# Performance work log

Hardware: AMD Instinct MI355X
Metric: run time of the kernel (lower is better)

Reference implementation:

```python
import jax, jax.numpy as jnp
import numpy as np

IN_F = 128
OUT_F = 128
GROUPS = 8
NUM_F = 8
B = 16
NP_ = 4096


def setup_inputs() -> dict:
    key = jax.random.key(0)
    ks = jax.random.split(key, 6)
    x = jax.random.normal(ks[0], (B, NP_, IN_F), dtype=jnp.float32)
    grid = jnp.arange(NUM_F, dtype=jnp.float32) + 1.0                      # [num_f]
    base_weight = jax.random.normal(ks[1], (OUT_F, IN_F), dtype=jnp.float32) * 0.05
    scale_sp = jnp.ones((OUT_F,), dtype=jnp.float32)
    coef = jax.random.uniform(ks[2], (GROUPS, 1, NUM_F), dtype=jnp.float32)
    conv_w = jax.random.normal(ks[3], (NUM_F, OUT_F, IN_F), dtype=jnp.float32) * 0.05  # grouped 1x1 conv
    conv_b = jax.random.normal(ks[4], (NUM_F, OUT_F), dtype=jnp.float32) * 0.05
    return {"x": x, "grid": grid, "base_weight": base_weight,
            "scale_sp": scale_sp, "coef": coef, "conv_w": conv_w, "conv_b": conv_b}


def reference(x, grid, base_weight, scale_sp, coef, conv_w, conv_b):
    Bd, Nd, D = x.shape
    num_f = grid.shape[0]
    groups = coef.shape[0]
    gsz = D // groups
    xf = x.reshape(Bd * Nd, D)                                  # [batch, in]
    # base path: SiLU then linear (no bias)
    base = jax.nn.silu(xf) @ base_weight.T                       # [batch, out]
    # spline path: sin(grid * x), broadcast coef per (group, f)
    s = jnp.sin(grid[None, :, None] * xf[:, None, :])            # [batch, num_f, in]
    cm = coef[:, 0, :].T                                         # [num_f, groups]
    s = s.reshape(-1, num_f, groups, gsz) * cm[None, :, :, None]
    s = s.reshape(-1, num_f, D)                                  # [batch, num_f, in]
    # grouped 1x1 conv == per-f GEMM
    spline = jnp.einsum('bfi,foi->bfo', s, conv_w) + conv_b[None]
    spline = spline.sum(axis=1) * scale_sp                       # [batch, out]
    out = (base + spline).reshape(Bd, Nd, -1)
    return out
```

## Files before the change

kernel.cpp:

```cpp
#include <hip/hip_runtime.h>
#include <hip/hip_bf16.h>
#include <stdint.h>

#define IN_F   128
#define OUT_F  128
#define NUM_F  8
#define NROWS  (16*4096)

typedef __bf16  bf16x8  __attribute__((ext_vector_type(8)));
typedef float   f32x16  __attribute__((ext_vector_type(16)));

#define WP_CHUNKS (9*8*4*64)
#define WP_BYTES  (WP_CHUNKS*16)
#define BIAS_OFF  WP_BYTES

__global__ __launch_bounds__(256) void skan_prep(
    const float* __restrict__ base_w,
    const float* __restrict__ scale,
    const float* __restrict__ coef,
    const float* __restrict__ conv_w,
    const float* __restrict__ conv_b,
    __bf16* __restrict__ Wp, float* __restrict__ bias)
{
    int gid = blockIdx.x * 256 + threadIdx.x;
    int l  = gid & 63;
    int t  = (gid >> 6) & 3;
    int s  = (gid >> 8) & 7;
    int fb = gid >> 11;
    int n  = t * 32 + (l & 31);
    int k0 = s * 16 + (l >> 5) * 8;
    __bf16* dst = Wp + (size_t)gid * 8;
    if (fb == 0) {
        #pragma unroll
        for (int j = 0; j < 8; ++j)
            dst[j] = (__bf16)base_w[n * IN_F + k0 + j];
    } else {
        int f = fb - 1;
        float sc = scale[n];
        #pragma unroll
        for (int j = 0; j < 8; ++j) {
            int k = k0 + j;
            float v = conv_w[((size_t)f * OUT_F + n) * IN_F + k]
                      * coef[(k >> 4) * NUM_F + f] * sc;
            dst[j] = (__bf16)v;
        }
    }
    if (gid < OUT_F) {
        float b = 0.f;
        #pragma unroll
        for (int f = 0; f < NUM_F; ++f) b += conv_b[f * OUT_F + gid];
        bias[gid] = b * scale[gid];
    }
}

__device__ __forceinline__ void gld_lds16(const void* g, void* l) {
    __builtin_amdgcn_global_load_lds(
        (const __attribute__((address_space(1))) uint32_t*)g,
        (__attribute__((address_space(3))) uint32_t*)l, 16, 0, 0);
}

__global__ __launch_bounds__(256, 2) void skan_main(
    const float* __restrict__ x,
    const __bf16* __restrict__ Wp,
    const float* __restrict__ bias,
    float* __restrict__ out)
{
    __shared__ uint4 smem4[2048];
    char* smem = (char*)smem4;

    const int tid = threadIdx.x;
    const int w   = tid >> 6;
    const int l   = tid & 63;
    const int hl  = l & 31;
    const int h   = l >> 5;
    const int m0  = blockIdx.x * 128 + w * 32;
    const int m   = m0 + hl;

    const float4* x4 = (const float4*)x + (size_t)m * (IN_F / 4) + 2 * h;
    float xe[64];
    #pragma unroll
    for (int s = 0; s < 8; ++s) {
        float4 a = x4[4 * s];
        float4 b = x4[4 * s + 1];
        xe[8*s+0] = a.x; xe[8*s+1] = a.y; xe[8*s+2] = a.z; xe[8*s+3] = a.w;
        xe[8*s+4] = b.x; xe[8*s+5] = b.y; xe[8*s+6] = b.z; xe[8*s+7] = b.w;
    }

    f32x16 acc[4];
    #pragma unroll
    for (int t = 0; t < 4; ++t)
        #pragma unroll
        for (int r = 0; r < 16; ++r) acc[t][r] = 0.f;

    const bf16x8* bp = (const bf16x8*)smem;
    const char* wpb  = (const char*)Wp;

    for (int fb = 0; fb < 9; ++fb) {
        __syncthreads();
        {
            const char* src = wpb + (size_t)fb * 32768;
            #pragma unroll
            for (int r = 0; r < 8; ++r) {
                int off = (r * 4 + w) * 1024;
                gld_lds16(src + off + l * 16, smem + off);
            }
        }
        bf16x8 af[8];
        if (fb == 0) {
            #pragma unroll
            for (int s = 0; s < 8; ++s)
                #pragma unroll
                for (int j = 0; j < 8; ++j) {
                    float v = xe[8*s+j];
                    float sv = v * __builtin_amdgcn_rcpf(1.0f + __expf(-v));
                    af[s][j] = (__bf16)sv;
                }
        } else {
            float cf = (float)fb * 0.15915494309189535f;
            #pragma unroll
            for (int s = 0; s < 8; ++s)
                #pragma unroll
                for (int j = 0; j < 8; ++j) {
                    float a = __builtin_amdgcn_fractf(cf * xe[8*s+j]);
                    af[s][j] = (__bf16)__builtin_amdgcn_sinf(a);
                }
        }
        __syncthreads();
        #pragma unroll
        for (int s = 0; s < 8; ++s) {
            #pragma unroll
            for (int t = 0; t < 4; ++t) {
                bf16x8 b = bp[(s * 4 + t) * 64 + l];
                acc[t] = __builtin_amdgcn_mfma_f32_32x32x16_bf16(af[s], b, acc[t], 0, 0, 0);
            }
        }
    }

    #pragma unroll
    for (int t = 0; t < 4; ++t) {
        float bv = bias[t * 32 + hl];
        #pragma unroll
        for (int r = 0; r < 16; ++r) {
            int row = (r & 3) + 8 * (r >> 2) + 4 * h;
            out[(size_t)(m0 + row) * OUT_F + t * 32 + hl] = acc[t][r] + bv;
        }
    }
}

extern "C" void kernel_launch(void* const* d_in, const int* in_sizes, int n_in,
                              void* d_out, int out_size, void* d_ws, size_t ws_size,
                              hipStream_t stream) {
    const float* x      = (const float*)d_in[0];
    const float* base_w = (const float*)d_in[2];
    const float* scale  = (const float*)d_in[3];
    const float* coef   = (const float*)d_in[4];
    const float* conv_w = (const float*)d_in[5];
    const float* conv_b = (const float*)d_in[6];
    __bf16* Wp   = (__bf16*)d_ws;
    float*  bias = (float*)((char*)d_ws + BIAS_OFF);
    float*  out  = (float*)d_out;

    skan_prep<<<WP_CHUNKS / 256, 256, 0, stream>>>(base_w, scale, coef, conv_w, conv_b, Wp, bias);
    skan_main<<<NROWS / 128, 256, 0, stream>>>(x, Wp, bias, out);
}
```

Measured before the change: 112.3 us.

## Double-buffer weight tiles in LDS and stage output through shared memory

Grows LDS to 64KB and double-buffers the per-feature weight tiles, so the next tile's global-to-LDS load and the next sin activation computation overlap with the current tile's MFMAs. This cuts one barrier per iteration. The epilogue now writes accumulators to LDS and then stores coalesced float4 rows instead of scattered scalar stores. The larger LDS footprint may lower occupancy below the two blocks per CU the launch bounds target.

```diff
diff --git a/kernel.cpp b/kernel.cpp
--- a/kernel.cpp
+++ b/kernel.cpp
@@ -65,8 +65,8 @@
     const float* __restrict__ bias,
     float* __restrict__ out)
 {
-    __shared__ uint4 smem4[2048];
-    char* smem = (char*)smem4;
+    __shared__ float smemf[16384];
+    char* smem = (char*)smemf;
 
     const int tid = threadIdx.x;
     const int w   = tid >> 6;
@@ -75,6 +75,15 @@
     const int h   = l >> 5;
     const int m0  = blockIdx.x * 128 + w * 32;
     const int m   = m0 + hl;
+
+    {
+        const char* src = (const char*)Wp;
+        #pragma unroll
+        for (int r = 0; r < 8; ++r) {
+            int off = (r * 4 + w) * 1024;
+            gld_lds16(src + off + l * 16, smem + off);
+        }
+    }
 
     const float4* x4 = (const float4*)x + (size_t)m * (IN_F / 4) + 2 * h;
     float xe[64];
@@ -86,37 +95,45 @@
         xe[8*s+4] = b.x; xe[8*s+5] = b.y; xe[8*s+6] = b.z; xe[8*s+7] = b.w;
     }
 
+    bf16x8 af[8];
+    #pragma unroll
+    for (int s = 0; s < 8; ++s)
+        #pragma unroll
+        for (int j = 0; j < 8; ++j) {
+            float v = xe[8*s+j];
+            float sv = v * __builtin_amdgcn_rcpf(1.0f + __expf(-v));
+            af[s][j] = (__bf16)sv;
+        }
+
     f32x16 acc[4];
     #pragma unroll
     for (int t = 0; t < 4; ++t)
         #pragma unroll
         for (int r = 0; r < 16; ++r) acc[t][r] = 0.f;
 
-    const bf16x8* bp = (const bf16x8*)smem;
-    const char* wpb  = (const char*)Wp;
+    __syncthreads();
 
     for (int fb = 0; fb < 9; ++fb) {
-        __syncthreads();
-        {
-            const char* src = wpb + (size_t)fb * 32768;
+        if (fb < 8) {
+            const char* src = (const char*)Wp + (size_t)(fb + 1) * 32768;
+            char* dst = smem + ((fb + 1) & 1) * 32768;
             #pragma unroll
             for (int r = 0; r < 8; ++r) {
                 int off = (r * 4 + w) * 1024;
-                gld_lds16(src + off + l * 16, smem + off);
+                gld_lds16(src + off + l * 16, dst + off);
             }
         }
-        bf16x8 af[8];
-        if (fb == 0) {
+        const bf16x8* bp = (const bf16x8*)(smem + (fb & 1) * 32768);
+        #pragma unroll
+        for (int s = 0; s < 8; ++s) {
             #pragma unroll
-            for (int s = 0; s < 8; ++s)
-                #pragma unroll
-                for (int j = 0; j < 8; ++j) {
-                    float v = xe[8*s+j];
-                    float sv = v * __builtin_amdgcn_rcpf(1.0f + __expf(-v));
-                    af[s][j] = (__bf16)sv;
-                }
-        } else {
-            float cf = (float)fb * 0.15915494309189535f;
+            for (int t = 0; t < 4; ++t) {
+                bf16x8 b = bp[(s * 4 + t) * 64 + l];
+                acc[t] = __builtin_amdgcn_mfma_f32_32x32x16_bf16(af[s], b, acc[t], 0, 0, 0);
+            }
+        }
+        if (fb < 8) {
+            float cf = (float)(fb + 1) * 0.15915494309189535f;
             #pragma unroll
             for (int s = 0; s < 8; ++s)
                 #pragma unroll
@@ -126,24 +143,24 @@
                 }
         }
         __syncthreads();
-        #pragma unroll
-        for (int s = 0; s < 8; ++s) {
-            #pragma unroll
-            for (int t = 0; t < 4; ++t) {
-                bf16x8 b = bp[(s * 4 + t) * 64 + l];
-                acc[t] = __builtin_amdgcn_mfma_f32_32x32x16_bf16(af[s], b, acc[t], 0, 0, 0);
-            }
-        }
     }
 
+    float* lw = (float*)(smem + w * 16384);
     #pragma unroll
     for (int t = 0; t < 4; ++t) {
         float bv = bias[t * 32 + hl];
         #pragma unroll
         for (int r = 0; r < 16; ++r) {
             int row = (r & 3) + 8 * (r >> 2) + 4 * h;
-            out[(size_t)(m0 + row) * OUT_F + t * 32 + hl] = acc[t][r] + bv;
+            lw[row * 128 + t * 32 + hl] = acc[t][r] + bv;
         }
+    }
+    float4* of4 = (float4*)out;
+    const float4* lw4 = (const float4*)lw;
+    #pragma unroll
+    for (int i = 0; i < 16; ++i) {
+        float4 v = lw4[i * 64 + l];
+        of4[(size_t)(m0 + 2 * i + h) * 32 + hl] = v;
     }
 }
 
```

New measurement: 113.7 us. No clear change (+1.3%).

## Double-buffer weight tiles in LDS and stage output through LDS

Applied to the files above, without the earlier changes.

Splits LDS into two 32 KB buffers so the next frequency block's weights load via global_load_lds while the current block's MFMAs run. This replaces the old load-then-sync-then-compute loop, which had two barriers per block. The sin/SiLU activation for each k-slice is now computed just before its MFMAs instead of building all eight fragments up front, which should cut register pressure. The epilogue writes accumulators into LDS and reads them back as row-contiguous float4 stores to global memory. The costs are twice the LDS per block, which may limit blocks per CU, and every wave redundantly loading the whole first tile.

```diff
diff --git a/kernel.cpp b/kernel.cpp
--- a/kernel.cpp
+++ b/kernel.cpp
@@ -59,14 +59,44 @@
         (__attribute__((address_space(3))) uint32_t*)l, 16, 0, 0);
 }
 
+#define STAGE(dstbuf, fbi)                                                    \
+    {                                                                         \
+        const char* _src = wpb + (size_t)(fbi) * 32768;                       \
+        _Pragma("unroll")                                                     \
+        for (int _r = 0; _r < 8; ++_r) {                                      \
+            int _off = (_r * 4 + w) * 1024 + l * 16;                          \
+            gld_lds16(_src + _off, (dstbuf) + _off);                          \
+        }                                                                     \
+    }
+
+#define FBODY(curbuf, fbi)                                                    \
+    {                                                                         \
+        const bf16x8* _bp = (const bf16x8*)(curbuf);                          \
+        float _cf = (float)(fbi) * 0.15915494309189535f;                      \
+        _Pragma("unroll")                                                     \
+        for (int _s = 0; _s < 8; ++_s) {                                      \
+            bf16x8 _af;                                                       \
+            _Pragma("unroll")                                                 \
+            for (int _j = 0; _j < 8; ++_j) {                                  \
+                float _a = __builtin_amdgcn_fractf(_cf * xe[8*_s+_j]);        \
+                _af[_j] = (__bf16)__builtin_amdgcn_sinf(_a);                  \
+            }                                                                 \
+            _Pragma("unroll")                                                 \
+            for (int _t = 0; _t < 4; ++_t) {                                  \
+                bf16x8 _b = _bp[(_s * 4 + _t) * 64 + l];                      \
+                acc[_t] = __builtin_amdgcn_mfma_f32_32x32x16_bf16(_af, _b, acc[_t], 0, 0, 0); \
+            }                                                                 \
+        }                                                                     \
+    }
+
 __global__ __launch_bounds__(256, 2) void skan_main(
     const float* __restrict__ x,
     const __bf16* __restrict__ Wp,
     const float* __restrict__ bias,
     float* __restrict__ out)
 {
-    __shared__ uint4 smem4[2048];
-    char* smem = (char*)smem4;
+    __shared__ __align__(16) char bufA[32768];
+    __shared__ __align__(16) char bufB[32768];
 
     const int tid = threadIdx.x;
     const int w   = tid >> 6;
@@ -76,12 +106,19 @@
     const int m0  = blockIdx.x * 128 + w * 32;
     const int m   = m0 + hl;
 
-    const float4* x4 = (const float4*)x + (size_t)m * (IN_F / 4) + 2 * h;
+    const char* wpb = (const char*)Wp;
+
+    #pragma unroll
+    for (int i = 0; i < 32; ++i)
+        gld_lds16(wpb + i * 1024 + l * 16, bufA + i * 1024 + l * 16);
+    STAGE(bufB, 1);
+
+    const float4* x4p = (const float4*)x + (size_t)m * (IN_F / 4) + 2 * h;
     float xe[64];
     #pragma unroll
     for (int s = 0; s < 8; ++s) {
-        float4 a = x4[4 * s];
-        float4 b = x4[4 * s + 1];
+        float4 a = x4p[4 * s];
+        float4 b = x4p[4 * s + 1];
         xe[8*s+0] = a.x; xe[8*s+1] = a.y; xe[8*s+2] = a.z; xe[8*s+3] = a.w;
         xe[8*s+4] = b.x; xe[8*s+5] = b.y; xe[8*s+6] = b.z; xe[8*s+7] = b.w;
     }
@@ -92,57 +129,56 @@
         #pragma unroll
         for (int r = 0; r < 16; ++r) acc[t][r] = 0.f;
 
-    const bf16x8* bp = (const bf16x8*)smem;
-    const char* wpb  = (const char*)Wp;
-
-    for (int fb = 0; fb < 9; ++fb) {
-        __syncthreads();
-        {
-            const char* src = wpb + (size_t)fb * 32768;
+    {
+        const bf16x8* bp = (const bf16x8*)bufA;
+        #pragma unroll
+        for (int s = 0; s < 8; ++s) {
+            bf16x8 af;
             #pragma unroll
-            for (int r = 0; r < 8; ++r) {
-                int off = (r * 4 + w) * 1024;
-                gld_lds16(src + off + l * 16, smem + off);
+            for (int j = 0; j < 8; ++j) {
+                float v = xe[8*s+j];
+                af[j] = (__bf16)(v * __builtin_amdgcn_rcpf(1.0f + __expf(-v)));
             }
-        }
-        bf16x8 af[8];
-        if (fb == 0) {
-            #pragma unroll
-            for (int s = 0; s < 8; ++s)
-                #pragma unroll
-                for (int j = 0; j < 8; ++j) {
-                    float v = xe[8*s+j];
-                    float sv = v * __builtin_amdgcn_rcpf(1.0f + __expf(-v));
-                    af[s][j] = (__bf16)sv;
-                }
-        } else {
-            float cf = (float)fb * 0.15915494309189535f;
-            #pragma unroll
-            for (int s = 0; s < 8; ++s)
-                #pragma unroll
-                for (int j = 0; j < 8; ++j) {
-                    float a = __builtin_amdgcn_fractf(cf * xe[8*s+j]);
-                    af[s][j] = (__bf16)__builtin_amdgcn_sinf(a);
-                }
-        }
-        __syncthreads();
-        #pragma unroll
-        for (int s = 0; s < 8; ++s) {
             #pragma unroll
             for (int t = 0; t < 4; ++t) {
                 bf16x8 b = bp[(s * 4 + t) * 64 + l];
-                acc[t] = __builtin_amdgcn_mfma_f32_32x32x16_bf16(af[s], b, acc[t], 0, 0, 0);
+                acc[t] = __builtin_amdgcn_mfma_f32_32x32x16_bf16(af, b, acc[t], 0, 0, 0);
             }
         }
     }
-
-    #pragma unroll
-    for (int t = 0; t < 4; ++t) {
-        float bv = bias[t * 32 + hl];
-        #pragma unroll
-        for (int r = 0; r < 16; ++r) {
-            int row = (r & 3) + 8 * (r >> 2) + 4 * h;
-            out[(size_t)(m0 + row) * OUT_F + t * 32 + hl] = acc[t][r] + bv;
+    __syncthreads();
+
+    #pragma unroll 1
+    for (int p = 0; p < 4; ++p) {
+        int fb = 2 * p + 1;
+        STAGE(bufA, fb + 1);
+        FBODY(bufB, fb);
+        __syncthreads();
+        if (p < 3) STAGE(bufB, fb + 2);
+        FBODY(bufA, fb + 1);
+        __syncthreads();
+    }
+
+    float*  lwf = (float*)(bufB + w * 8192);
+    float4* lw4 = (float4*)lwf;
+    float4* of4 = (float4*)out;
+    #pragma unroll
+    for (int p = 0; p < 2; ++p) {
+        #pragma unroll
+        for (int tt = 0; tt < 2; ++tt) {
+            int t = 2 * p + tt;
+            float bv = bias[t * 32 + hl];
+            #pragma unroll
+            for (int r = 0; r < 16; ++r) {
+                int row = (r & 3) + 8 * (r >> 2) + 4 * h;
+                lwf[row * 64 + tt * 32 + hl] = acc[t][r] + bv;
+            }
+        }
+        #pragma unroll
+        for (int i = 0; i < 8; ++i) {
+            float4 v = lw4[i * 64 + l];
+            int row = i * 4 + (l >> 4);
+            of4[(size_t)(m0 + row) * 32 + p * 16 + (l & 15)] = v;
         }
     }
 }
```

New measurement: 113.3 us. About the same (+1.0%).

## Split output columns per block, keep weights resident in LDS, use sine recurrence

Applied to the files above, without the earlier changes.

Each block now handles 256 rows and one half of the output columns, loading that half's full 9-slice weight set into LDS once instead of streaming it per slice with barriers. x is held packed as bf16 in registers to save VGPRs, and sin(f·x) for f=1..8 comes from the Chebyshev recurrence sin((f+1)x)=2cos(x)sin(fx)-sin((f-1)x), which replaces seven extra sin evaluations with FMAs. The trade-offs are: x is read twice (once per column half), x is rounded to bf16 before the activations, the recurrence builds up error across f, and occupancy drops to one block per CU given the large LDS footprint. The prep kernel's spline branch applies the same coef factor to all 8 values of a chunk, which is valid because 8-element chunks never cross a 16-wide group.

```diff
diff --git a/kernel.cpp b/kernel.cpp
--- a/kernel.cpp
+++ b/kernel.cpp
@@ -10,7 +10,8 @@
 typedef __bf16  bf16x8  __attribute__((ext_vector_type(8)));
 typedef float   f32x16  __attribute__((ext_vector_type(16)));
 
-#define WP_CHUNKS (9*8*4*64)
+#define LDS_HALF  (9*8*2*64*16)
+#define WP_CHUNKS (2*9*8*2*64)
 #define WP_BYTES  (WP_CHUNKS*16)
 #define BIAS_OFF  WP_BYTES
 
@@ -23,27 +24,30 @@
     __bf16* __restrict__ Wp, float* __restrict__ bias)
 {
     int gid = blockIdx.x * 256 + threadIdx.x;
-    int l  = gid & 63;
-    int t  = (gid >> 6) & 3;
-    int s  = (gid >> 8) & 7;
-    int fb = gid >> 11;
-    int n  = t * 32 + (l & 31);
+    int flat = gid;
+    int l  = flat & 63;  flat >>= 6;
+    int t2 = flat & 1;   flat >>= 1;
+    int s  = flat & 7;   flat >>= 3;
+    int fb = flat % 9;
+    int h2 = flat / 9;
+    int n  = h2 * 64 + t2 * 32 + (l & 31);
     int k0 = s * 16 + (l >> 5) * 8;
     __bf16* dst = Wp + (size_t)gid * 8;
     if (fb == 0) {
-        #pragma unroll
-        for (int j = 0; j < 8; ++j)
-            dst[j] = (__bf16)base_w[n * IN_F + k0 + j];
+        const float4* b4 = (const float4*)(base_w + n * IN_F + k0);
+        float4 a = b4[0], b = b4[1];
+        dst[0]=(__bf16)a.x; dst[1]=(__bf16)a.y; dst[2]=(__bf16)a.z; dst[3]=(__bf16)a.w;
+        dst[4]=(__bf16)b.x; dst[5]=(__bf16)b.y; dst[6]=(__bf16)b.z; dst[7]=(__bf16)b.w;
     } else {
         int f = fb - 1;
         float sc = scale[n];
-        #pragma unroll
-        for (int j = 0; j < 8; ++j) {
-            int k = k0 + j;
-            float v = conv_w[((size_t)f * OUT_F + n) * IN_F + k]
-                      * coef[(k >> 4) * NUM_F + f] * sc;
-            dst[j] = (__bf16)v;
-        }
+        const float4* c4 = (const float4*)(conv_w + ((size_t)f * OUT_F + n) * IN_F + k0);
+        float4 a = c4[0], b = c4[1];
+        float m0c = coef[((k0    ) >> 4) * NUM_F + f] * sc;
+        float m1c = coef[((k0 + 4) >> 4) * NUM_F + f] * sc;
+        (void)m1c;
+        dst[0]=(__bf16)(a.x*m0c); dst[1]=(__bf16)(a.y*m0c); dst[2]=(__bf16)(a.z*m0c); dst[3]=(__bf16)(a.w*m0c);
+        dst[4]=(__bf16)(b.x*m0c); dst[5]=(__bf16)(b.y*m0c); dst[6]=(__bf16)(b.z*m0c); dst[7]=(__bf16)(b.w*m0c);
     }
     if (gid < OUT_F) {
         float b = 0.f;
@@ -59,90 +63,146 @@
         (__attribute__((address_space(3))) uint32_t*)l, 16, 0, 0);
 }
 
-__global__ __launch_bounds__(256, 2) void skan_main(
+__device__ __forceinline__ uint32_t pkbf(float a, float b) {
+    __bf16 x = (__bf16)a, y = (__bf16)b;
+    uint16_t ux, uy;
+    __builtin_memcpy(&ux, &x, 2);
+    __builtin_memcpy(&uy, &y, 2);
+    return (uint32_t)ux | ((uint32_t)uy << 16);
+}
+__device__ __forceinline__ float upk_lo(uint32_t p) { return __uint_as_float(p << 16); }
+__device__ __forceinline__ float upk_hi(uint32_t p) { return __uint_as_float(p & 0xffff0000u); }
+
+__global__ __launch_bounds__(256, 1) void skan_main(
     const float* __restrict__ x,
     const __bf16* __restrict__ Wp,
     const float* __restrict__ bias,
     float* __restrict__ out)
 {
-    __shared__ uint4 smem4[2048];
-    char* smem = (char*)smem4;
-
-    const int tid = threadIdx.x;
-    const int w   = tid >> 6;
-    const int l   = tid & 63;
-    const int hl  = l & 31;
-    const int h   = l >> 5;
-    const int m0  = blockIdx.x * 128 + w * 32;
-    const int m   = m0 + hl;
-
-    const float4* x4 = (const float4*)x + (size_t)m * (IN_F / 4) + 2 * h;
-    float xe[64];
+    __shared__ __align__(16) char sB[LDS_HALF];
+
+    const int tid  = threadIdx.x;
+    const int w    = tid >> 6;
+    const int l    = tid & 63;
+    const int hl   = l & 31;
+    const int h    = l >> 5;
+    const int bx   = blockIdx.x;
+    const int half = bx & 1;
+    const int m0   = (bx >> 1) * 256 + w * 64;
+
+    const char* src = (const char*)Wp + (size_t)half * LDS_HALF;
+    #pragma unroll
+    for (int i = 0; i < 36; ++i) {
+        int off = (i * 256 + tid) * 16;
+        gld_lds16(src + off, sB + off);
+    }
+
+    const float4* x4 = (const float4*)x;
+    uint32_t xe[2][32];
+    #pragma unroll
+    for (int g = 0; g < 2; ++g) {
+        size_t base = (size_t)(m0 + 32 * g + hl) * 32 + 2 * h;
+        #pragma unroll
+        for (int s = 0; s < 8; ++s) {
+            float4 a = x4[base + 4 * s];
+            float4 b = x4[base + 4 * s + 1];
+            xe[g][4*s+0] = pkbf(a.x, a.y);
+            xe[g][4*s+1] = pkbf(a.z, a.w);
+            xe[g][4*s+2] = pkbf(b.x, b.y);
+            xe[g][4*s+3] = pkbf(b.z, b.w);
+        }
+    }
+
+    f32x16 acc[2][2];
+    #pragma unroll
+    for (int g = 0; g < 2; ++g)
+        #pragma unroll
+        for (int t = 0; t < 2; ++t)
+            #pragma unroll
+            for (int r = 0; r < 16; ++r) acc[g][t][r] = 0.f;
+
+    __syncthreads();
+
+    const bf16x8* bp = (const bf16x8*)sB;
+
     #pragma unroll
     for (int s = 0; s < 8; ++s) {
-        float4 a = x4[4 * s];
-        float4 b = x4[4 * s + 1];
-        xe[8*s+0] = a.x; xe[8*s+1] = a.y; xe[8*s+2] = a.z; xe[8*s+3] = a.w;
-        xe[8*s+4] = b.x; xe[8*s+5] = b.y; xe[8*s+6] = b.z; xe[8*s+7] = b.w;
-    }
-
-    f32x16 acc[4];
-    #pragma unroll
-    for (int t = 0; t < 4; ++t)
-        #pragma unroll
-        for (int r = 0; r < 16; ++r) acc[t][r] = 0.f;
-
-    const bf16x8* bp = (const bf16x8*)smem;
-    const char* wpb  = (const char*)Wp;
-
-    for (int fb = 0; fb < 9; ++fb) {
-        __syncthreads();
-        {
-            const char* src = wpb + (size_t)fb * 32768;
-            #pragma unroll
-            for (int r = 0; r < 8; ++r) {
-                int off = (r * 4 + w) * 1024;
-                gld_lds16(src + off + l * 16, smem + off);
-            }
-        }
-        bf16x8 af[8];
-        if (fb == 0) {
-            #pragma unroll
-            for (int s = 0; s < 8; ++s)
+        bf16x8 a0, a1;
+        #pragma unroll
+        for (int g = 0; g < 2; ++g) {
+            #pragma unroll
+            for (int jp = 0; jp < 4; ++jp) {
+                uint32_t p = xe[g][4*s+jp];
+                float lo = upk_lo(p), hi = upk_hi(p);
+                float slo = lo * __builtin_amdgcn_rcpf(1.0f + __expf(-lo));
+                float shi = hi * __builtin_amdgcn_rcpf(1.0f + __expf(-hi));
+                if (g == 0) { a0[2*jp] = (__bf16)slo; a0[2*jp+1] = (__bf16)shi; }
+                else        { a1[2*jp] = (__bf16)slo; a1[2*jp+1] = (__bf16)shi; }
+            }
+        }
+        #pragma unroll
+        for (int t = 0; t < 2; ++t) {
+            bf16x8 b = bp[(s * 2 + t) * 64 + l];
+            acc[0][t] = __builtin_amdgcn_mfma_f32_32x32x16_bf16(a0, b, acc[0][t], 0, 0, 0);
+            acc[1][t] = __builtin_amdgcn_mfma_f32_32x32x16_bf16(a1, b, acc[1][t], 0, 0, 0);
+        }
+    }
+
+    #pragma unroll
+    for (int s = 0; s < 8; ++s) {
+        float sp[16], sp2[16], tc[16];
+        #pragma unroll
+        for (int g = 0; g < 2; ++g) {
+            #pragma unroll
+            for (int jp = 0; jp < 4; ++jp) {
+                uint32_t p = xe[g][4*s+jp];
+                float lo = upk_lo(p), hi = upk_hi(p);
+                float rl = __builtin_amdgcn_fractf(lo * 0.15915494309189535f);
+                float rh = __builtin_amdgcn_fractf(hi * 0.15915494309189535f);
+                int j0 = g * 8 + 2 * jp;
+                sp[j0]     = __builtin_amdgcn_sinf(rl);
+                sp[j0+1]   = __builtin_amdgcn_sinf(rh);
+                tc[j0]     = 2.0f * __builtin_amdgcn_cosf(rl);
+                tc[j0+1]   = 2.0f * __builtin_amdgcn_cosf(rh);
+                sp2[j0]    = 0.0f;
+                sp2[j0+1]  = 0.0f;
+            }
+        }
+        #pragma unroll
+        for (int f = 1; f <= 8; ++f) {
+            bf16x8 a0, a1;
+            #pragma unroll
+            for (int j = 0; j < 8; ++j) {
+                a0[j] = (__bf16)sp[j];
+                a1[j] = (__bf16)sp[8 + j];
+            }
+            #pragma unroll
+            for (int t = 0; t < 2; ++t) {
+                bf16x8 b = bp[((f * 8 + s) * 2 + t) * 64 + l];
+                acc[0][t] = __builtin_amdgcn_mfma_f32_32x32x16_bf16(a0, b, acc[0][t], 0, 0, 0);
+                acc[1][t] = __builtin_amdgcn_mfma_f32_32x32x16_bf16(a1, b, acc[1][t], 0, 0, 0);
+            }
+            if (f < 8) {
                 #pragma unroll
-                for (int j = 0; j < 8; ++j) {
-                    float v = xe[8*s+j];
-                    float sv = v * __builtin_amdgcn_rcpf(1.0f + __expf(-v));
-                    af[s][j] = (__bf16)sv;
+                for (int i = 0; i < 16; ++i) {
+                    float sn = __builtin_fmaf(tc[i], sp[i], -sp2[i]);
+                    sp2[i] = sp[i];
+                    sp[i]  = sn;
                 }
-        } else {
-            float cf = (float)fb * 0.15915494309189535f;
-            #pragma unroll
-            for (int s = 0; s < 8; ++s)
-                #pragma unroll
-                for (int j = 0; j < 8; ++j) {
-                    float a = __builtin_amdgcn_fractf(cf * xe[8*s+j]);
-                    af[s][j] = (__bf16)__builtin_amdgcn_sinf(a);
-                }
-        }
-        __syncthreads();
-        #pragma unroll
-        for (int s = 0; s < 8; ++s) {
-            #pragma unroll
-            for (int t = 0; t < 4; ++t) {
-                bf16x8 b = bp[(s * 4 + t) * 64 + l];
-                acc[t] = __builtin_amdgcn_mfma_f32_32x32x16_bf16(af[s], b, acc[t], 0, 0, 0);
-            }
-        }
-    }
-
-    #pragma unroll
-    for (int t = 0; t < 4; ++t) {
-        float bv = bias[t * 32 + hl];
-        #pragma unroll
-        for (int r = 0; r < 16; ++r) {
-            int row = (r & 3) + 8 * (r >> 2) + 4 * h;
-            out[(size_t)(m0 + row) * OUT_F + t * 32 + hl] = acc[t][r] + bv;
+            }
+        }
+    }
+
+    #pragma unroll
+    for (int g = 0; g < 2; ++g) {
+        #pragma unroll
+        for (int t = 0; t < 2; ++t) {
+            float bv = bias[half * 64 + t * 32 + hl];
+            #pragma unroll
+            for (int r = 0; r < 16; ++r) {
+                int row = (r & 3) + 8 * (r >> 2) + 4 * h + 32 * g;
+                out[(size_t)(m0 + row) * OUT_F + half * 64 + t * 32 + hl] = acc[g][t][r] + bv;
+            }
         }
     }
 }
@@ -161,5 +221,5 @@
     float*  out  = (float*)d_out;
 
     skan_prep<<<WP_CHUNKS / 256, 256, 0, stream>>>(base_w, scale, coef, conv_w, conv_b, Wp, bias);
-    skan_main<<<NROWS / 128, 256, 0, stream>>>(x, Wp, bias, out);
-}
+    skan_main<<<(NROWS / 256) * 2, 256, 0, stream>>>(x, Wp, bias, out);
+}
```

After: 119.7 us. 1.07x slower.
